# Performance work log

Measured on AMD Instinct MI355X. Metric: run time of the kernel, lower is better.

Reference implementation:

```python
import jax, jax.numpy as jnp
import numpy as np

NUM_PROJS = 7
BLOCK = 32

def _gray_perm(n):
    # unit-hamming-distance (Gray-code) permutation used by AngularLSH
    a = np.array([0, 1], dtype=np.int32)
    for s in range(2, n + 1):
        a = np.concatenate([a, a[::-1] + 2 ** (s - 1)])
    return a

PERM = jnp.asarray(_gray_perm(NUM_PROJS))
ENC = jnp.asarray(2 ** np.arange(NUM_PROJS), dtype=np.int32)  # [R]


def lsh_hash(x, proj_dir):
    # x: [B,H,S,D], proj_dir: [D,R] -> integer bucket ids [B,H,S]
    bits = (jnp.einsum('bhsd,dr->bhsr', x, proj_dir) > 0).astype(jnp.int32)
    code = (bits * ENC).sum(-1)
    return PERM[code]


def sdpa(q, k, v, mask):
    # q,k,v: [...,S,D]; mask: bool broadcastable to [...,Sq,Sk]
    scale = q.shape[-1] ** -0.5
    scores = jnp.einsum('...qd,...kd->...qk', q, k) * scale
    scores = jnp.where(mask, scores, -jnp.inf)
    return jnp.einsum('...qk,...kd->...qd', jax.nn.softmax(scores, axis=-1), v)


def setup_inputs() -> dict:
    key = jax.random.key(0)
    kq, kk, kv, kp = jax.random.split(key, 4)
    B, H, S, D = 2, 16, 2048, 128
    return {
        'q': jax.random.normal(kq, (B, H, S, D), dtype=jnp.float32),
        'k': jax.random.normal(kk, (B, H, S, D), dtype=jnp.float32),
        'v': jax.random.normal(kv, (B, H, S, D), dtype=jnp.float32),
        'proj_dir': jax.random.normal(kp, (D, NUM_PROJS), dtype=jnp.float32),
        'mask': jnp.ones((1, 1, 1, 1), dtype=bool),
    }


def reference(q, k, v, proj_dir, mask):
    B, H, S, D = q.shape
    # 1) LSH hash queries, stable sort along seq dim, reorder queries
    q_hash = lsh_hash(q, proj_dir)                                   # [B,H,S]
    sort_idx = jnp.argsort(q_hash, axis=2, stable=True)              # [B,H,S]
    q_hash_sorted = jnp.take_along_axis(q_hash, sort_idx, axis=2)
    q_sorted = jnp.take_along_axis(q, sort_idx[..., None], axis=2)   # [B,H,S,D]
    # 2) hash keys (unsorted), split into blocks of size BLOCK
    k_hash = lsh_hash(k, proj_dir)                                   # [B,H,S]
    k_hash_blk = k_hash.reshape(-1, 1, BLOCK)                        # [NB,1,32]
    q_hash_blk = q_hash_sorted.reshape(-1, 1, BLOCK)
    # 3) criticality: per-block count of matching hash ids; critical blocks get K zeroed
    criticality = (k_hash_blk == q_hash_blk).sum(-1).squeeze(-1)     # [NB]
    keep = (criticality <= 0).astype(q.dtype)                        # 0 where critical (matches torch loop)
    Qb = q_sorted.reshape(-1, 1, BLOCK, D)                           # [NB,1,32,D]
    Kb = k.reshape(-1, 1, BLOCK, D) * keep[:, None, None, None]
    Vb = v.reshape(-1, 1, BLOCK, D)
    # 4) dual SDPA: blocked critical attention + full dense attention
    out_critical = sdpa(Qb, Kb, Vb, mask).reshape(B, H, S, D)
    out_actual = sdpa(q, k, v, mask)                                 # [B,H,S,D]
    loss = jnp.mean((out_critical - out_actual) ** 2)
    return out_actual, loss
```

## Files before the change

kernel.cpp:

```cpp
#include <hip/hip_runtime.h>
#include <hip/hip_bf16.h>

#define SEQ 2048
#define DIM 128
#define NBH 32
#define NROWS (NBH*SEQ)
#define NBLK (NROWS/32)
#define SCALE 0.08838834764831845f
#define QSC (0.08838834764831845f * 1.4426950408889634f)

typedef __attribute__((ext_vector_type(8))) short short8;
typedef __attribute__((ext_vector_type(16))) float float16;

__device__ __forceinline__ unsigned short f2bf(float x) {
    union { float f; unsigned u; } v; v.f = x;
    unsigned r = v.u + 0x7fffu + ((v.u >> 16) & 1u);
    return (unsigned short)(r >> 16);
}
__device__ __forceinline__ unsigned pack_bf16(float a, float b) {
    float2 f; f.x = a; f.y = b;
    __hip_bfloat162 h = __float22bfloat162_rn(f);
    union { __hip_bfloat162 h2; unsigned u; } cv; cv.h2 = h; return cv.u;
}
__device__ __forceinline__ void gl_lds16(const void* g, void* l) {
    __builtin_amdgcn_global_load_lds((const __attribute__((address_space(1))) unsigned int*)g,
                                     (__attribute__((address_space(3))) unsigned int*)l, 16, 0, 0);
}

__global__ __launch_bounds__(256) void hash_kernel(const float* __restrict__ qg, const float* __restrict__ kg,
                            const float* __restrict__ proj,
                            int* __restrict__ qh, int* __restrict__ kh)
{
    const int gw   = (int)((blockIdx.x * blockDim.x + threadIdx.x) >> 6);
    const int lane = threadIdx.x & 63;
    const int sub  = lane >> 4;
    const int dl   = (lane & 15) * 8;
    const int r    = gw * 4 + sub;
    const float* src; int* dst; int row;
    if (r < NROWS) { src = qg; dst = qh; row = r; }
    else           { src = kg; dst = kh; row = r - NROWS; }

    const float* x = src + (size_t)row * DIM + dl;
    float xv[8];
    {
        float4 f0 = *(const float4*)x;
        float4 f1 = *(const float4*)(x + 4);
        xv[0]=f0.x; xv[1]=f0.y; xv[2]=f0.z; xv[3]=f0.w;
        xv[4]=f1.x; xv[5]=f1.y; xv[6]=f1.z; xv[7]=f1.w;
    }
    float pj[56];
    #pragma unroll
    for (int i = 0; i < 14; ++i)
        *(float4*)&pj[i*4] = *(const float4*)(proj + dl*7 + i*4);

    float a[7] = {0.f,0.f,0.f,0.f,0.f,0.f,0.f};
    #pragma unroll
    for (int d = 0; d < 8; ++d)
        #pragma unroll
        for (int p = 0; p < 7; ++p) a[p] = fmaf(xv[d], pj[d*7+p], a[p]);

    #pragma unroll
    for (int off = 1; off < 16; off <<= 1)
        #pragma unroll
        for (int p = 0; p < 7; ++p) a[p] += __shfl_xor(a[p], off, 64);

    if ((lane & 15) == 0) {
        int code = 0;
        if (a[0] > 0.f) code |= 1;  if (a[1] > 0.f) code |= 2;
        if (a[2] > 0.f) code |= 4;  if (a[3] > 0.f) code |= 8;
        if (a[4] > 0.f) code |= 16; if (a[5] > 0.f) code |= 32;
        if (a[6] > 0.f) code |= 64;
        dst[row] = code ^ (code >> 1);
    }
}

__global__ __launch_bounds__(256) void sort_kernel(const int* __restrict__ qh,
                                                   int* __restrict__ sidx, int* __restrict__ qhs)
{
    __shared__ unsigned short cnt[128][260];
    __shared__ int startv[128];
    const int bh = blockIdx.x;
    const int t  = threadIdx.x;
    const int base = bh*SEQ;

    for (int i = t; i < 128*260; i += 256) ((unsigned short*)cnt)[i] = 0;
    __syncthreads();

    int hv[8];
    {
        int4 a = *(const int4*)(qh + base + t*8);
        int4 b = *(const int4*)(qh + base + t*8 + 4);
        hv[0]=a.x; hv[1]=a.y; hv[2]=a.z; hv[3]=a.w;
        hv[4]=b.x; hv[5]=b.y; hv[6]=b.z; hv[7]=b.w;
    }
    #pragma unroll
    for (int i = 0; i < 8; ++i) cnt[hv[i]][t]++;
    __syncthreads();

    const int wv = t >> 6, l = t & 63;
    #pragma unroll 1
    for (int v = wv; v < 128; v += 4) {
        ushort4 cc = *(const ushort4*)&cnt[v][4*l];
        unsigned c0 = cc.x, c1 = cc.y, c2 = cc.z, c3 = cc.w;
        unsigned s01 = c0 + c1;
        unsigned s = s01 + c2 + c3;
        unsigned inc = s;
        #pragma unroll
        for (int off = 1; off < 64; off <<= 1) {
            unsigned o = __shfl_up(inc, off, 64);
            if (l >= off) inc += o;
        }
        unsigned ex = inc - s;
        ushort4 wb;
        wb.x = (unsigned short)ex;
        wb.y = (unsigned short)(ex + c0);
        wb.z = (unsigned short)(ex + s01);
        wb.w = (unsigned short)(ex + s01 + c2);
        *(ushort4*)&cnt[v][4*l] = wb;
        if (l == 63) cnt[v][256] = (unsigned short)inc;
    }
    __syncthreads();

    if (t < 64) {
        int a0 = cnt[2*t][256], a1 = cnt[2*t+1][256];
        int s2 = a0 + a1, inc = s2;
        #pragma unroll
        for (int off = 1; off < 64; off <<= 1) {
            int o = __shfl_up(inc, off, 64);
            if (t >= off) inc += o;
        }
        int ex = inc - s2;
        startv[2*t]   = ex;
        startv[2*t+1] = ex + a0;
    }
    __syncthreads();

    #pragma unroll
    for (int i = 0; i < 8; ++i) {
        const int v = hv[i];
        int prior = 0;
        #pragma unroll
        for (int j = 0; j < 8; ++j) if (j < i && hv[j] == v) ++prior;
        const int rank = startv[v] + (int)cnt[v][t] + prior;
        sidx[base + rank] = t*8 + i;
        qhs[base + rank]  = v;
    }
}

__global__ __launch_bounds__(256) void prep_kernel(const float* __restrict__ kg,
                                                   const float* __restrict__ vg,
                                                   unsigned short* __restrict__ kbf,
                                                   unsigned short* __restrict__ vtg)
{
    __shared__ unsigned short T[128][72];
    const int t  = threadIdx.x;
    const int h  = blockIdx.x >> 5;
    const int sl = blockIdx.x & 31;
    const size_t base = ((size_t)h*SEQ + sl*64) * DIM;

    #pragma unroll
    for (int i = 0; i < 8; ++i) {
        const float4 f = *(const float4*)(kg + base + ((size_t)i*256 + t)*4);
        uint2 pk; pk.x = pack_bf16(f.x, f.y); pk.y = pack_bf16(f.z, f.w);
        *(uint2*)(kbf + base + ((size_t)i*256 + t)*4) = pk;
    }

    const int kk = t & 63, seg = t >> 6;
    #pragma unroll
    for (int i = 0; i < 8; ++i) {
        float4 f = *(const float4*)(vg + base + (size_t)kk*DIM + seg*32 + i*4);
        T[seg*32 + i*4 + 0][kk] = f2bf(f.x);
        T[seg*32 + i*4 + 1][kk] = f2bf(f.y);
        T[seg*32 + i*4 + 2][kk] = f2bf(f.z);
        T[seg*32 + i*4 + 3][kk] = f2bf(f.w);
    }
    __syncthreads();
    const int r = t >> 1, hf = t & 1;
    unsigned short* dst = vtg + ((size_t)h*DIM + r)*SEQ + sl*64 + hf*32;
    #pragma unroll
    for (int i = 0; i < 4; ++i)
        *(short8*)(dst + i*8) = *(const short8*)&T[r][hf*32 + i*8];
}

__global__ __launch_bounds__(256, 2) void dense_attn_mfma(
    const unsigned short* __restrict__ kbf, const unsigned short* __restrict__ vtg,
    const float* __restrict__ qg, float* __restrict__ outg)
{
    __shared__ __align__(16) unsigned short KbF[2*8192];
    __shared__ __align__(16) unsigned short VbF[2*8192];

    const int t    = threadIdx.x;
    const int lane = t & 63;
    const int w    = t >> 6;
    const int q5   = lane >> 5;
    const int l31  = lane & 31;
    const int e    = l31 & 7;

    const int b    = blockIdx.x;
    const int slot = b >> 3;
    const int head = (b & 7) * 4 + (slot >> 4);
    const int qblk = slot & 15;

    const float* Qg = qg + ((size_t)head*SEQ + qblk*128 + w*32) * DIM;
    const unsigned short* Kh = kbf + (size_t)head*SEQ*DIM;
    const unsigned short* Vh = vtg + (size_t)head*DIM*SEQ;

    int koff[8], voff[4];
    #pragma unroll
    for (int ch = 0; ch < 8; ++ch) koff[ch] = l31*128 + (((2*ch + q5) ^ e) * 8);
    #pragma unroll
    for (int u = 0; u < 4; ++u)    voff[u]  = l31*64  + ((((u>>1)*4 + (u&1)*2 + q5) ^ e) * 8);

    const unsigned short* kgp[4]; unsigned short* kls[4];
    const unsigned short* vgp[4]; unsigned short* vls[4];
    #pragma unroll
    for (int i = 0; i < 4; ++i) {
        const int j = w*4 + i;
        const int r = j*4 + (lane >> 4);
        const int u = (lane & 15) ^ (r & 7);
        kgp[i] = Kh + r*DIM + u*8;
        kls[i] = KbF + j*512;
        const int d = j*8 + (lane >> 3);
        const int u2 = (lane & 7) ^ (d & 7);
        vgp[i] = Vh + (size_t)d*SEQ + u2*8;
        vls[i] = VbF + j*512;
    }

    auto stage = [&](const int buf) {
        #pragma unroll
        for (int i = 0; i < 4; ++i) gl_lds16(kgp[i], kls[i] + buf*8192);
        #pragma unroll
        for (int i = 0; i < 4; ++i) gl_lds16(vgp[i], vls[i] + buf*8192);
        #pragma unroll
        for (int i = 0; i < 4; ++i) { kgp[i] += 8192; vgp[i] += 64; }
    };

    stage(0);

    union FR { unsigned u[4]; short8 s; };
    short8 Qf[8];
    #pragma unroll
    for (int ch = 0; ch < 8; ++ch) {
        const float* p = Qg + (size_t)l31*DIM + ch*16 + q5*8;
        float4 f0 = *(const float4*)p;
        float4 f1 = *(const float4*)(p + 4);
        FR fr;
        fr.u[0] = pack_bf16(f0.x*QSC, f0.y*QSC);
        fr.u[1] = pack_bf16(f0.z*QSC, f0.w*QSC);
        fr.u[2] = pack_bf16(f1.x*QSC, f1.y*QSC);
        fr.u[3] = pack_bf16(f1.z*QSC, f1.w*QSC);
        Qf[ch] = fr.s;
    }

    float16 o[4];
    #pragma unroll
    for (int mt = 0; mt < 4; ++mt)
        #pragma unroll
        for (int r = 0; r < 16; ++r) o[mt][r] = 0.f;
    float lsum0 = 0.f, lsum1 = 0.f;

    auto body = [&](const int buf) {
        #pragma unroll
        for (int s = 0; s < 2; ++s) {
            float16 sv, sw;
            #pragma unroll
            for (int r = 0; r < 16; ++r) { sv[r] = 0.f; sw[r] = 0.f; }
            __builtin_amdgcn_s_setprio(1);
            #pragma unroll
            for (int ch = 0; ch < 4; ++ch) {
                short8 kf = *(const short8*)&KbF[buf*8192 + s*4096 + koff[ch]];
                sv = __builtin_amdgcn_mfma_f32_32x32x16_bf16(kf, Qf[ch], sv, 0, 0, 0);
                short8 kg2 = *(const short8*)&KbF[buf*8192 + s*4096 + koff[ch+4]];
                sw = __builtin_amdgcn_mfma_f32_32x32x16_bf16(kg2, Qf[ch+4], sw, 0, 0, 0);
            }
            __builtin_amdgcn_s_setprio(0);
            unsigned pk[8];
            #pragma unroll
            for (int rp = 0; rp < 8; ++rp) {
                float p0 = __builtin_amdgcn_exp2f(sv[2*rp]   + sw[2*rp]);
                float p1 = __builtin_amdgcn_exp2f(sv[2*rp+1] + sw[2*rp+1]);
                lsum0 += p0; lsum1 += p1;
                pk[rp] = pack_bf16(p0, p1);
            }
            unsigned e0 = __shfl_xor(q5 ? pk[0] : pk[2], 32, 64);
            unsigned e1 = __shfl_xor(q5 ? pk[1] : pk[3], 32, 64);
            unsigned e2 = __shfl_xor(q5 ? pk[4] : pk[6], 32, 64);
            unsigned e3 = __shfl_xor(q5 ? pk[5] : pk[7], 32, 64);
            FR c0, c1;
            if (q5 == 0) {
                c0.u[0]=pk[0]; c0.u[1]=pk[1]; c0.u[2]=e0;    c0.u[3]=e1;
                c1.u[0]=pk[4]; c1.u[1]=pk[5]; c1.u[2]=e2;    c1.u[3]=e3;
            } else {
                c0.u[0]=e0;    c0.u[1]=e1;    c0.u[2]=pk[2]; c0.u[3]=pk[3];
                c1.u[0]=e2;    c1.u[1]=e3;    c1.u[2]=pk[6]; c1.u[3]=pk[7];
            }
            __builtin_amdgcn_s_setprio(1);
            #pragma unroll
            for (int c = 0; c < 2; ++c) {
                short8 pf = c ? c1.s : c0.s;
                #pragma unroll
                for (int mt = 0; mt < 4; ++mt) {
                    short8 vf = *(const short8*)&VbF[buf*8192 + mt*2048 + voff[s*2 + c]];
                    o[mt] = __builtin_amdgcn_mfma_f32_32x32x16_bf16(vf, pf, o[mt], 0, 0, 0);
                }
            }
            __builtin_amdgcn_s_setprio(0);
        }
    };

    #pragma unroll 2
    for (int kt = 0; kt < 32; ++kt) {
        asm volatile("s_waitcnt vmcnt(0) lgkmcnt(0)" ::: "memory");
        __builtin_amdgcn_s_barrier();
        if (kt < 31) stage((kt & 1) ^ 1);
        body(kt & 1);
    }

    const float lsum = lsum0 + lsum1;
    const float l = lsum + __shfl_xor(lsum, 32, 64);
    const float inv = 1.f / l;
    float* orow = outg + ((size_t)head*SEQ + qblk*128 + w*32 + l31) * DIM;
    #pragma unroll
    for (int mt = 0; mt < 4; ++mt)
        #pragma unroll
        for (int rg = 0; rg < 4; ++rg) {
            const int d0 = mt*32 + rg*8 + q5*4;
            float4 ov;
            ov.x = o[mt][rg*4+0]*inv; ov.y = o[mt][rg*4+1]*inv;
            ov.z = o[mt][rg*4+2]*inv; ov.w = o[mt][rg*4+3]*inv;
            *(float4*)(orow + d0) = ov;
        }
}

__global__ __launch_bounds__(256) void crit_attn(
    const unsigned short* __restrict__ kbf, const unsigned short* __restrict__ vtg,
    const float* __restrict__ qg, const int* __restrict__ sidx,
    const int* __restrict__ kh, const int* __restrict__ qhs,
    const float* __restrict__ outg, float* __restrict__ lossp)
{
    __shared__ float wsum[4];
    const int t    = threadIdx.x;
    const int lane = t & 63;
    const int w    = t >> 6;
    const int nb   = blockIdx.x * 4 + w;
    const int q5   = lane >> 5;
    const int l31  = lane & 31;
    const int bh   = nb >> 6;

    const int khv = kh[nb*32 + l31];
    const int qhv = qhs[nb*32 + l31];
    const unsigned long long mm = __ballot(khv == qhv);
    const float kp = ((mm & 0xffffffffull) == 0ull) ? 1.0f : 0.0f;

    const int qrow = sidx[bh*SEQ + (nb & 63)*32 + l31];

    union FR { unsigned u[4]; short8 s; };
    short8 Qf[8];
    const float* Qg = qg + ((size_t)bh*SEQ + qrow) * DIM;
    #pragma unroll
    for (int ch = 0; ch < 8; ++ch) {
        const float* p = Qg + ch*16 + q5*8;
        float4 f0 = *(const float4*)p;
        float4 f1 = *(const float4*)(p + 4);
        FR fr;
        fr.u[0] = pack_bf16(f0.x*QSC, f0.y*QSC);
        fr.u[1] = pack_bf16(f0.z*QSC, f0.w*QSC);
        fr.u[2] = pack_bf16(f1.x*QSC, f1.y*QSC);
        fr.u[3] = pack_bf16(f1.z*QSC, f1.w*QSC);
        Qf[ch] = fr.s;
    }

    const unsigned short* Kb = kbf + (size_t)(nb*32) * DIM;
    float16 sv, sw;
    #pragma unroll
    for (int r = 0; r < 16; ++r) { sv[r] = 0.f; sw[r] = 0.f; }
    #pragma unroll
    for (int ch = 0; ch < 4; ++ch) {
        short8 kf = *(const short8*)(Kb + (size_t)l31*DIM + ch*16 + q5*8);
        sv = __builtin_amdgcn_mfma_f32_32x32x16_bf16(kf, Qf[ch], sv, 0, 0, 0);
        short8 kg2 = *(const short8*)(Kb + (size_t)l31*DIM + (ch+4)*16 + q5*8);
        sw = __builtin_amdgcn_mfma_f32_32x32x16_bf16(kg2, Qf[ch+4], sw, 0, 0, 0);
    }

    float lsum = 0.f;
    unsigned pk[8];
    #pragma unroll
    for (int rp = 0; rp < 8; ++rp) {
        float p0 = __builtin_amdgcn_exp2f((sv[2*rp]   + sw[2*rp])   * kp);
        float p1 = __builtin_amdgcn_exp2f((sv[2*rp+1] + sw[2*rp+1]) * kp);
        lsum += p0 + p1;
        pk[rp] = pack_bf16(p0, p1);
    }
    unsigned e0 = __shfl_xor(q5 ? pk[0] : pk[2], 32, 64);
    unsigned e1 = __shfl_xor(q5 ? pk[1] : pk[3], 32, 64);
    unsigned e2 = __shfl_xor(q5 ? pk[4] : pk[6], 32, 64);
    unsigned e3 = __shfl_xor(q5 ? pk[5] : pk[7], 32, 64);
    FR c0, c1;
    if (q5 == 0) {
        c0.u[0]=pk[0]; c0.u[1]=pk[1]; c0.u[2]=e0;    c0.u[3]=e1;
        c1.u[0]=pk[4]; c1.u[1]=pk[5]; c1.u[2]=e2;    c1.u[3]=e3;
    } else {
        c0.u[0]=e0;    c0.u[1]=e1;    c0.u[2]=pk[2]; c0.u[3]=pk[3];
        c1.u[0]=e2;    c1.u[1]=e3;    c1.u[2]=pk[6]; c1.u[3]=pk[7];
    }
    const float ltot = lsum + __shfl_xor(lsum, 32, 64);

    const unsigned short* Vb = vtg + (size_t)bh*DIM*SEQ + (size_t)(nb & 63)*32;
    float16 o[4];
    #pragma unroll
    for (int mt = 0; mt < 4; ++mt)
        #pragma unroll
        for (int r = 0; r < 16; ++r) o[mt][r] = 0.f;
    #pragma unroll
    for (int c = 0; c < 2; ++c) {
        short8 pf = c ? c1.s : c0.s;
        #pragma unroll
        for (int mt = 0; mt < 4; ++mt) {
            short8 vf = *(const short8*)(Vb + (size_t)(mt*32 + l31)*SEQ + c*16 + q5*8);
            o[mt] = __builtin_amdgcn_mfma_f32_32x32x16_bf16(vf, pf, o[mt], 0, 0, 0);
        }
    }

    const float inv = 1.f / ltot;
    const float* oa_row = outg + (size_t)(nb*32 + l31) * DIM;
    float sq = 0.f;
    #pragma unroll
    for (int mt = 0; mt < 4; ++mt)
        #pragma unroll
        for (int rg = 0; rg < 4; ++rg) {
            const int d0 = mt*32 + rg*8 + q5*4;
            float4 oa = *(const float4*)(oa_row + d0);
            float dx = o[mt][rg*4+0]*inv - oa.x;
            float dy = o[mt][rg*4+1]*inv - oa.y;
            float dz = o[mt][rg*4+2]*inv - oa.z;
            float dw = o[mt][rg*4+3]*inv - oa.w;
            sq += dx*dx + dy*dy + dz*dz + dw*dw;
        }
    #pragma unroll
    for (int off = 32; off > 0; off >>= 1) sq += __shfl_down(sq, off, 64);
    if (lane == 0) wsum[w] = sq;
    __syncthreads();
    if (t == 0) atomicAdd(lossp, (wsum[0]+wsum[1]+wsum[2]+wsum[3]) * (1.0f/8388608.0f));
}

extern "C" void kernel_launch(void* const* d_in, const int* in_sizes, int n_in,
                              void* d_out, int out_size, void* d_ws, size_t ws_size,
                              hipStream_t stream)
{
    const float* q    = (const float*)d_in[0];
    const float* k    = (const float*)d_in[1];
    const float* v    = (const float*)d_in[2];
    const float* proj = (const float*)d_in[3];
    float* out   = (float*)d_out;
    float* lossp = out + (out_size - 1);

    int* qh   = (int*)d_ws;
    int* kh   = qh + NROWS;
    int* sidx = kh + NROWS;
    int* qhs  = sidx + NROWS;
    unsigned short* kbf = (unsigned short*)(qhs + NROWS);
    unsigned short* vtg = kbf + (size_t)NROWS*DIM;

    hipMemsetAsync(lossp, 0, sizeof(float), stream);
    prep_kernel<<<NBH*32, 256, 0, stream>>>(k, v, kbf, vtg);
    hash_kernel<<<(2*NROWS)/16, 256, 0, stream>>>(q, k, proj, qh, kh);
    sort_kernel<<<NBH, 256, 0, stream>>>(qh, sidx, qhs);
    dense_attn_mfma<<<512, 256, 0, stream>>>(kbf, vtg, q, out);
    crit_attn<<<NBLK/4, 256, 0, stream>>>(kbf, vtg, q, sidx, kh, qhs, out, lossp);
}
```

Measured before the change: 285.6 us.

## Process two 32-row query tiles per wave to reuse K/V LDS fragments

Each wave now handles 64 query rows (two 32-row MFMA tiles) instead of 32, so every K and V fragment read from LDS feeds two MFMAs. The grid is halved to 256 blocks with a 256-row query block per workgroup, and launch bounds drop to one block per CU. The K/V stage loop is restructured into an explicit double-buffered pair with __syncthreads instead of a manual waitcnt plus barrier. This trades higher register pressure and lower occupancy, with 256 blocks possibly underfilling the CUs, for halved LDS and global K/V traffic per query.

Result: slower. 317.7 us (+11.2%).

```diff
diff --git a/kernel.cpp b/kernel.cpp
--- a/kernel.cpp
+++ b/kernel.cpp
@@ -182,7 +182,7 @@
         *(short8*)(dst + i*8) = *(const short8*)&T[r][hf*32 + i*8];
 }
 
-__global__ __launch_bounds__(256, 2) void dense_attn_mfma(
+__global__ __launch_bounds__(256, 1) void dense_attn_mfma(
     const unsigned short* __restrict__ kbf, const unsigned short* __restrict__ vtg,
     const float* __restrict__ qg, float* __restrict__ outg)
 {
@@ -197,11 +197,10 @@
     const int e    = l31 & 7;
 
     const int b    = blockIdx.x;
-    const int slot = b >> 3;
-    const int head = (b & 7) * 4 + (slot >> 4);
-    const int qblk = slot & 15;
-
-    const float* Qg = qg + ((size_t)head*SEQ + qblk*128 + w*32) * DIM;
+    const int head = (b & 7) * 4 + (b >> 6);
+    const int qblk = (b >> 3) & 7;
+
+    const float* Qg = qg + ((size_t)head*SEQ + qblk*256 + w*64) * DIM;
     const unsigned short* Kh = kbf + (size_t)head*SEQ*DIM;
     const unsigned short* Vh = vtg + (size_t)head*DIM*SEQ;
 
@@ -238,97 +237,125 @@
     stage(0);
 
     union FR { unsigned u[4]; short8 s; };
-    short8 Qf[8];
+    short8 QfA[8], QfB[8];
     #pragma unroll
     for (int ch = 0; ch < 8; ++ch) {
-        const float* p = Qg + (size_t)l31*DIM + ch*16 + q5*8;
-        float4 f0 = *(const float4*)p;
-        float4 f1 = *(const float4*)(p + 4);
-        FR fr;
-        fr.u[0] = pack_bf16(f0.x*QSC, f0.y*QSC);
-        fr.u[1] = pack_bf16(f0.z*QSC, f0.w*QSC);
-        fr.u[2] = pack_bf16(f1.x*QSC, f1.y*QSC);
-        fr.u[3] = pack_bf16(f1.z*QSC, f1.w*QSC);
-        Qf[ch] = fr.s;
-    }
-
-    float16 o[4];
+        const float* pA = Qg + (size_t)l31*DIM + ch*16 + q5*8;
+        const float* pB = pA + (size_t)32*DIM;
+        float4 a0 = *(const float4*)pA;
+        float4 a1 = *(const float4*)(pA + 4);
+        float4 b0 = *(const float4*)pB;
+        float4 b1 = *(const float4*)(pB + 4);
+        FR fa, fb;
+        fa.u[0] = pack_bf16(a0.x*QSC, a0.y*QSC);
+        fa.u[1] = pack_bf16(a0.z*QSC, a0.w*QSC);
+        fa.u[2] = pack_bf16(a1.x*QSC, a1.y*QSC);
+        fa.u[3] = pack_bf16(a1.z*QSC, a1.w*QSC);
+        fb.u[0] = pack_bf16(b0.x*QSC, b0.y*QSC);
+        fb.u[1] = pack_bf16(b0.z*QSC, b0.w*QSC);
+        fb.u[2] = pack_bf16(b1.x*QSC, b1.y*QSC);
+        fb.u[3] = pack_bf16(b1.z*QSC, b1.w*QSC);
+        QfA[ch] = fa.s;
+        QfB[ch] = fb.s;
+    }
+
+    float16 oA[4], oB[4];
     #pragma unroll
     for (int mt = 0; mt < 4; ++mt)
         #pragma unroll
-        for (int r = 0; r < 16; ++r) o[mt][r] = 0.f;
-    float lsum0 = 0.f, lsum1 = 0.f;
+        for (int r = 0; r < 16; ++r) { oA[mt][r] = 0.f; oB[mt][r] = 0.f; }
+    float lsumA = 0.f, lsumB = 0.f;
 
     auto body = [&](const int buf) {
         #pragma unroll
         for (int s = 0; s < 2; ++s) {
-            float16 sv, sw;
+            float16 svA, svB;
             #pragma unroll
-            for (int r = 0; r < 16; ++r) { sv[r] = 0.f; sw[r] = 0.f; }
+            for (int r = 0; r < 16; ++r) { svA[r] = 0.f; svB[r] = 0.f; }
             __builtin_amdgcn_s_setprio(1);
             #pragma unroll
-            for (int ch = 0; ch < 4; ++ch) {
+            for (int ch = 0; ch < 8; ++ch) {
                 short8 kf = *(const short8*)&KbF[buf*8192 + s*4096 + koff[ch]];
-                sv = __builtin_amdgcn_mfma_f32_32x32x16_bf16(kf, Qf[ch], sv, 0, 0, 0);
-                short8 kg2 = *(const short8*)&KbF[buf*8192 + s*4096 + koff[ch+4]];
-                sw = __builtin_amdgcn_mfma_f32_32x32x16_bf16(kg2, Qf[ch+4], sw, 0, 0, 0);
+                svA = __builtin_amdgcn_mfma_f32_32x32x16_bf16(kf, QfA[ch], svA, 0, 0, 0);
+                svB = __builtin_amdgcn_mfma_f32_32x32x16_bf16(kf, QfB[ch], svB, 0, 0, 0);
             }
             __builtin_amdgcn_s_setprio(0);
-            unsigned pk[8];
+            unsigned pkA[8], pkB[8];
             #pragma unroll
             for (int rp = 0; rp < 8; ++rp) {
-                float p0 = __builtin_amdgcn_exp2f(sv[2*rp]   + sw[2*rp]);
-                float p1 = __builtin_amdgcn_exp2f(sv[2*rp+1] + sw[2*rp+1]);
-                lsum0 += p0; lsum1 += p1;
-                pk[rp] = pack_bf16(p0, p1);
+                float a0 = __builtin_amdgcn_exp2f(svA[2*rp]);
+                float a1 = __builtin_amdgcn_exp2f(svA[2*rp+1]);
+                float b0 = __builtin_amdgcn_exp2f(svB[2*rp]);
+                float b1 = __builtin_amdgcn_exp2f(svB[2*rp+1]);
+                lsumA += a0 + a1;
+                lsumB += b0 + b1;
+                pkA[rp] = pack_bf16(a0, a1);
+                pkB[rp] = pack_bf16(b0, b1);
             }
-            unsigned e0 = __shfl_xor(q5 ? pk[0] : pk[2], 32, 64);
-            unsigned e1 = __shfl_xor(q5 ? pk[1] : pk[3], 32, 64);
-            unsigned e2 = __shfl_xor(q5 ? pk[4] : pk[6], 32, 64);
-            unsigned e3 = __shfl_xor(q5 ? pk[5] : pk[7], 32, 64);
-            FR c0, c1;
+            unsigned eA0 = __shfl_xor(q5 ? pkA[0] : pkA[2], 32, 64);
+            unsigned eA1 = __shfl_xor(q5 ? pkA[1] : pkA[3], 32, 64);
+            unsigned eA2 = __shfl_xor(q5 ? pkA[4] : pkA[6], 32, 64);
+            unsigned eA3 = __shfl_xor(q5 ? pkA[5] : pkA[7], 32, 64);
+            unsigned eB0 = __shfl_xor(q5 ? pkB[0] : pkB[2], 32, 64);
+            unsigned eB1 = __shfl_xor(q5 ? pkB[1] : pkB[3], 32, 64);
+            unsigned eB2 = __shfl_xor(q5 ? pkB[4] : pkB[6], 32, 64);
+            unsigned eB3 = __shfl_xor(q5 ? pkB[5] : pkB[7], 32, 64);
+            FR cA0, cA1, cB0, cB1;
             if (q5 == 0) {
-                c0.u[0]=pk[0]; c0.u[1]=pk[1]; c0.u[2]=e0;    c0.u[3]=e1;
-                c1.u[0]=pk[4]; c1.u[1]=pk[5]; c1.u[2]=e2;    c1.u[3]=e3;
+                cA0.u[0]=pkA[0]; cA0.u[1]=pkA[1]; cA0.u[2]=eA0;    cA0.u[3]=eA1;
+                cA1.u[0]=pkA[4]; cA1.u[1]=pkA[5]; cA1.u[2]=eA2;    cA1.u[3]=eA3;
+                cB0.u[0]=pkB[0]; cB0.u[1]=pkB[1]; cB0.u[2]=eB0;    cB0.u[3]=eB1;
+                cB1.u[0]=pkB[4]; cB1.u[1]=pkB[5]; cB1.u[2]=eB2;    cB1.u[3]=eB3;
             } else {
-                c0.u[0]=e0;    c0.u[1]=e1;    c0.u[2]=pk[2]; c0.u[3]=pk[3];
-                c1.u[0]=e2;    c1.u[1]=e3;    c1.u[2]=pk[6]; c1.u[3]=pk[7];
+                cA0.u[0]=eA0;    cA0.u[1]=eA1;    cA0.u[2]=pkA[2]; cA0.u[3]=pkA[3];
+                cA1.u[0]=eA2;    cA1.u[1]=eA3;    cA1.u[2]=pkA[6]; cA1.u[3]=pkA[7];
+                cB0.u[0]=eB0;    cB0.u[1]=eB1;    cB0.u[2]=pkB[2]; cB0.u[3]=pkB[3];
+                cB1.u[0]=eB2;    cB1.u[1]=eB3;    cB1.u[2]=pkB[6]; cB1.u[3]=pkB[7];
             }
             __builtin_amdgcn_s_setprio(1);
             #pragma unroll
             for (int c = 0; c < 2; ++c) {
-                short8 pf = c ? c1.s : c0.s;
+                short8 pfA = c ? cA1.s : cA0.s;
+                short8 pfB = c ? cB1.s : cB0.s;
                 #pragma unroll
                 for (int mt = 0; mt < 4; ++mt) {
                     short8 vf = *(const short8*)&VbF[buf*8192 + mt*2048 + voff[s*2 + c]];
-                    o[mt] = __builtin_amdgcn_mfma_f32_32x32x16_bf16(vf, pf, o[mt], 0, 0, 0);
+                    oA[mt] = __builtin_amdgcn_mfma_f32_32x32x16_bf16(vf, pfA, oA[mt], 0, 0, 0);
+                    oB[mt] = __builtin_amdgcn_mfma_f32_32x32x16_bf16(vf, pfB, oB[mt], 0, 0, 0);
                 }
             }
             __builtin_amdgcn_s_setprio(0);
         }
     };
 
-    #pragma unroll 2
-    for (int kt = 0; kt < 32; ++kt) {
-        asm volatile("s_waitcnt vmcnt(0) lgkmcnt(0)" ::: "memory");
-        __builtin_amdgcn_s_barrier();
-        if (kt < 31) stage((kt & 1) ^ 1);
-        body(kt & 1);
-    }
-
-    const float lsum = lsum0 + lsum1;
-    const float l = lsum + __shfl_xor(lsum, 32, 64);
-    const float inv = 1.f / l;
-    float* orow = outg + ((size_t)head*SEQ + qblk*128 + w*32 + l31) * DIM;
+    #pragma unroll 1
+    for (int kt2 = 0; kt2 < 16; ++kt2) {
+        __syncthreads();
+        stage(1);
+        body(0);
+        __syncthreads();
+        if (kt2 < 15) stage(0);
+        body(1);
+    }
+
+    const float lA = lsumA + __shfl_xor(lsumA, 32, 64);
+    const float lB = lsumB + __shfl_xor(lsumB, 32, 64);
+    const float invA = 1.f / lA;
+    const float invB = 1.f / lB;
+    float* orowA = outg + ((size_t)head*SEQ + qblk*256 + w*64 + l31) * DIM;
+    float* orowB = orowA + (size_t)32*DIM;
     #pragma unroll
     for (int mt = 0; mt < 4; ++mt)
         #pragma unroll
         for (int rg = 0; rg < 4; ++rg) {
             const int d0 = mt*32 + rg*8 + q5*4;
-            float4 ov;
-            ov.x = o[mt][rg*4+0]*inv; ov.y = o[mt][rg*4+1]*inv;
-            ov.z = o[mt][rg*4+2]*inv; ov.w = o[mt][rg*4+3]*inv;
-            *(float4*)(orow + d0) = ov;
+            float4 oa, ob;
+            oa.x = oA[mt][rg*4+0]*invA; oa.y = oA[mt][rg*4+1]*invA;
+            oa.z = oA[mt][rg*4+2]*invA; oa.w = oA[mt][rg*4+3]*invA;
+            ob.x = oB[mt][rg*4+0]*invB; ob.y = oB[mt][rg*4+1]*invB;
+            ob.z = oB[mt][rg*4+2]*invB; ob.w = oB[mt][rg*4+3]*invB;
+            *(float4*)(orowA + d0) = oa;
+            *(float4*)(orowB + d0) = ob;
         }
 }
 
@@ -465,6 +492,6 @@
     prep_kernel<<<NBH*32, 256, 0, stream>>>(k, v, kbf, vtg);
     hash_kernel<<<(2*NROWS)/16, 256, 0, stream>>>(q, k, proj, qh, kh);
     sort_kernel<<<NBH, 256, 0, stream>>>(qh, sidx, qhs);
-    dense_attn_mfma<<<512, 256, 0, stream>>>(kbf, vtg, q, out);
+    dense_attn_mfma<<<256, 256, 0, stream>>>(kbf, vtg, q, out);
     crit_attn<<<NBLK/4, 256, 0, stream>>>(kbf, vtg, q, sidx, kh, qhs, out, lossp);
 }
```

## Store K/V tiles in fragment-major LDS layout and simplify dense attention loop

Applied to the files above, without the earlier changes.

Changes the LDS staging layout of K and V tiles so each lane reads its MFMA fragment from a contiguous lane*8 offset, removing the XOR swizzle offset tables. The QK product now uses a single accumulator chain over 8 chunks instead of two interleaved chains, and the s_setprio hints are dropped. The main loop is rewritten as an explicit double-buffer pair with __syncthreads instead of manual waitcnt plus barrier. The contiguous layout may create LDS bank conflicts, and the single MFMA dependency chain reduces instruction-level parallelism.

Result: no change. 289.9 us (+1.5%).

```diff
diff --git a/kernel.cpp b/kernel.cpp
--- a/kernel.cpp
+++ b/kernel.cpp
@@ -194,7 +194,7 @@
     const int w    = t >> 6;
     const int q5   = lane >> 5;
     const int l31  = lane & 31;
-    const int e    = l31 & 7;
+    const int lvec = lane * 8;
 
     const int b    = blockIdx.x;
     const int slot = b >> 3;
@@ -205,25 +205,18 @@
     const unsigned short* Kh = kbf + (size_t)head*SEQ*DIM;
     const unsigned short* Vh = vtg + (size_t)head*DIM*SEQ;
 
-    int koff[8], voff[4];
-    #pragma unroll
-    for (int ch = 0; ch < 8; ++ch) koff[ch] = l31*128 + (((2*ch + q5) ^ e) * 8);
-    #pragma unroll
-    for (int u = 0; u < 4; ++u)    voff[u]  = l31*64  + ((((u>>1)*4 + (u&1)*2 + q5) ^ e) * 8);
-
     const unsigned short* kgp[4]; unsigned short* kls[4];
     const unsigned short* vgp[4]; unsigned short* vls[4];
-    #pragma unroll
-    for (int i = 0; i < 4; ++i) {
-        const int j = w*4 + i;
-        const int r = j*4 + (lane >> 4);
-        const int u = (lane & 15) ^ (r & 7);
-        kgp[i] = Kh + r*DIM + u*8;
-        kls[i] = KbF + j*512;
-        const int d = j*8 + (lane >> 3);
-        const int u2 = (lane & 7) ^ (d & 7);
-        vgp[i] = Vh + (size_t)d*SEQ + u2*8;
-        vls[i] = VbF + j*512;
+    {
+        const int ks = w >> 1, vs = w >> 1, vc = w & 1;
+        #pragma unroll
+        for (int i = 0; i < 4; ++i) {
+            const int kch = (w & 1) * 4 + i;
+            kgp[i] = Kh + (size_t)(ks*32 + l31)*DIM + kch*16 + q5*8;
+            kls[i] = KbF + (ks*8 + kch)*512;
+            vgp[i] = Vh + (size_t)(i*32 + l31)*SEQ + vs*32 + vc*16 + q5*8;
+            vls[i] = VbF + (vs*8 + vc*4 + i)*512;
+        }
     }
 
     auto stage = [&](const int buf) {
@@ -257,29 +250,26 @@
     for (int mt = 0; mt < 4; ++mt)
         #pragma unroll
         for (int r = 0; r < 16; ++r) o[mt][r] = 0.f;
-    float lsum0 = 0.f, lsum1 = 0.f;
+    float lsum = 0.f;
 
     auto body = [&](const int buf) {
+        const int B = buf*8192;
         #pragma unroll
         for (int s = 0; s < 2; ++s) {
-            float16 sv, sw;
+            float16 sv;
             #pragma unroll
-            for (int r = 0; r < 16; ++r) { sv[r] = 0.f; sw[r] = 0.f; }
-            __builtin_amdgcn_s_setprio(1);
+            for (int r = 0; r < 16; ++r) sv[r] = 0.f;
             #pragma unroll
-            for (int ch = 0; ch < 4; ++ch) {
-                short8 kf = *(const short8*)&KbF[buf*8192 + s*4096 + koff[ch]];
+            for (int ch = 0; ch < 8; ++ch) {
+                short8 kf = *(const short8*)&KbF[B + s*4096 + ch*512 + lvec];
                 sv = __builtin_amdgcn_mfma_f32_32x32x16_bf16(kf, Qf[ch], sv, 0, 0, 0);
-                short8 kg2 = *(const short8*)&KbF[buf*8192 + s*4096 + koff[ch+4]];
-                sw = __builtin_amdgcn_mfma_f32_32x32x16_bf16(kg2, Qf[ch+4], sw, 0, 0, 0);
             }
-            __builtin_amdgcn_s_setprio(0);
             unsigned pk[8];
             #pragma unroll
             for (int rp = 0; rp < 8; ++rp) {
-                float p0 = __builtin_amdgcn_exp2f(sv[2*rp]   + sw[2*rp]);
-                float p1 = __builtin_amdgcn_exp2f(sv[2*rp+1] + sw[2*rp+1]);
-                lsum0 += p0; lsum1 += p1;
+                float p0 = __builtin_amdgcn_exp2f(sv[2*rp]);
+                float p1 = __builtin_amdgcn_exp2f(sv[2*rp+1]);
+                lsum += p0 + p1;
                 pk[rp] = pack_bf16(p0, p1);
             }
             unsigned e0 = __shfl_xor(q5 ? pk[0] : pk[2], 32, 64);
@@ -294,29 +284,28 @@
                 c0.u[0]=e0;    c0.u[1]=e1;    c0.u[2]=pk[2]; c0.u[3]=pk[3];
                 c1.u[0]=e2;    c1.u[1]=e3;    c1.u[2]=pk[6]; c1.u[3]=pk[7];
             }
-            __builtin_amdgcn_s_setprio(1);
             #pragma unroll
             for (int c = 0; c < 2; ++c) {
                 short8 pf = c ? c1.s : c0.s;
                 #pragma unroll
                 for (int mt = 0; mt < 4; ++mt) {
-                    short8 vf = *(const short8*)&VbF[buf*8192 + mt*2048 + voff[s*2 + c]];
+                    short8 vf = *(const short8*)&VbF[B + s*4096 + c*2048 + mt*512 + lvec];
                     o[mt] = __builtin_amdgcn_mfma_f32_32x32x16_bf16(vf, pf, o[mt], 0, 0, 0);
                 }
             }
-            __builtin_amdgcn_s_setprio(0);
         }
     };
 
-    #pragma unroll 2
-    for (int kt = 0; kt < 32; ++kt) {
-        asm volatile("s_waitcnt vmcnt(0) lgkmcnt(0)" ::: "memory");
-        __builtin_amdgcn_s_barrier();
-        if (kt < 31) stage((kt & 1) ^ 1);
-        body(kt & 1);
-    }
-
-    const float lsum = lsum0 + lsum1;
+    #pragma unroll 1
+    for (int kt2 = 0; kt2 < 16; ++kt2) {
+        __syncthreads();
+        stage(1);
+        body(0);
+        __syncthreads();
+        if (kt2 < 15) stage(0);
+        body(1);
+    }
+
     const float l = lsum + __shfl_xor(lsum, 32, 64);
     const float inv = 1.f / l;
     float* orow = outg + ((size_t)head*SEQ + qblk*128 + w*32 + l31) * DIM;
```
